# Kernel tuning notes

Hardware: AMD Instinct MI355X
Metric: run time of the kernel (lower is better)

Reference implementation:

```python
import jax, jax.numpy as jnp
import numpy as np

N_CELLS = 500_000
B = 512
D_X = 128
D_Z = 32
D_IN = D_X + D_Z  # 160
H = 256
D_OUT = 16


def _linear_params(key, fan_in, fan_out):
    k1, k2 = jax.random.split(key)
    bound = 1.0 / np.sqrt(fan_in)
    W = jax.random.uniform(k1, (fan_in, fan_out), jnp.float32, -bound, bound)
    b = jax.random.uniform(k2, (fan_out,), jnp.float32, -bound, bound)
    return W, b


def setup_inputs() -> dict:
    key = jax.random.key(0)
    ks = jax.random.split(key, 8)
    X = jax.random.uniform(ks[0], (N_CELLS, D_X), jnp.float32)  # nonneg counts-like
    Z = jax.random.normal(ks[1], (B, D_Z), jnp.float32)
    cell_to_batch = jax.random.randint(ks[2], (N_CELLS,), 0, B, jnp.int64)
    sample_idx_batch = jnp.arange(B, dtype=jnp.int64)
    W1, b1 = _linear_params(ks[3], D_IN, H)
    W2, b2 = _linear_params(ks[4], H, H)
    W3, b3 = _linear_params(ks[5], H, D_OUT)
    return {"X": X, "Z": Z, "W1": W1, "b1": b1, "W2": W2, "b2": b2,
            "W3": W3, "b3": b3, "cell_to_batch": cell_to_batch,
            "sample_idx_batch": sample_idx_batch}


def reference(X, Z, W1, b1, W2, b2, W3, b3, cell_to_batch, sample_idx_batch):
    # gather per-sample covariates to per-cell rows
    Zc = Z[cell_to_batch]                              # [N, D_Z]
    seg = sample_idx_batch[cell_to_batch]              # [N] remapped sample ids
    # preprocessor: log-normalize X, concat covariates
    Xp = jnp.concatenate([jnp.log1p(X), Zc], axis=-1)  # [N, D_IN]
    # cell predictor MLP (Linear-ReLU x2 + Linear)
    h = jax.nn.relu(Xp @ W1 + b1)
    h = jax.nn.relu(h @ W2 + b2)
    X_cell = h @ W3 + b3                               # [N, D_OUT]
    # aggregator: segment mean over cells of each sample
    nseg = sample_idx_batch.shape[0]
    sums = jax.ops.segment_sum(X_cell, seg, num_segments=nseg)
    counts = jax.ops.segment_sum(jnp.ones((X_cell.shape[0], 1), X_cell.dtype), seg, num_segments=nseg)
    Y_sample = sums / jnp.maximum(counts, 1.0)
    # postprocessor: identity
    return Y_sample
```

## Files before the change

kernel.cpp:

```cpp
#include <hip/hip_runtime.h>
#include <hip/hip_bf16.h>

typedef __attribute__((ext_vector_type(8))) short short8;
typedef __attribute__((ext_vector_type(4))) short short4v;
typedef __attribute__((ext_vector_type(4))) float floatx4;

#define N_CELLS  500000
#define B_SAMP   512
#define D_X      128
#define D_Z      32
#define H_DIM    256
#define D_OUT    16

#define M_TILE   128
#define NBLK     3907
#define LDH      264
#define SP_LD    20

#define NREP     64

#define OFF_W1P   0
#define OFF_W2P   65536
#define OFF_W3P   196608
#define OFF_ZW    204800
#define OFF_ACC   729088
#define OFF_CNT   2826240
#define OFF_C2S   2957312

#define W1_BLKS   128
#define W2_BLKS   256
#define W3_BLKS   16
#define ZW_BLKS   512
#define C2S_BLKS  1954

__device__ __forceinline__ short bfb(float x) {
    union { __hip_bfloat16 h; short s; } u;
    u.h = __float2bfloat16(x);
    return u.s;
}
__device__ __forceinline__ int pack2(float a, float b) {
    return ((int)(unsigned short)bfb(a)) | ((int)bfb(b) << 16);
}

__global__ __launch_bounds__(256)
void prep(const float* __restrict__ W1, const float* __restrict__ b1,
          const float* __restrict__ W2, const float* __restrict__ W3,
          const float* __restrict__ Z,
          const int* __restrict__ c2b, const int* __restrict__ sidx,
          __hip_bfloat16* __restrict__ w1p, __hip_bfloat16* __restrict__ w2p,
          __hip_bfloat16* __restrict__ w3p, float* __restrict__ zw1,
          float* __restrict__ cnts, int* __restrict__ c2s) {
    int bid = blockIdx.x;
    int tid = threadIdx.x;
    if (bid < W1_BLKS + W2_BLKS + W3_BLKS) {
        const float* W; __hip_bfloat16* dst; int N, kS, idx; float scale;
        if (bid < W1_BLKS) {
            idx = bid * 256 + tid; W = W1; dst = w1p; N = H_DIM; kS = 4;
            scale = 0.6931471805599453f;
        } else if (bid < W1_BLKS + W2_BLKS) {
            idx = (bid - W1_BLKS) * 256 + tid; W = W2; dst = w2p; N = H_DIM; kS = 8;
            scale = 1.0f;
        } else {
            idx = (bid - W1_BLKS - W2_BLKS) * 256 + tid; W = W3; dst = w3p; N = D_OUT; kS = 8;
            scale = 1.0f;
        }
        int j = idx & 7;
        int L = (idx >> 3) & 63;
        int s = (idx >> 9) % kS;
        int t = idx / (kS << 9);
        int k = s * 32 + ((L >> 4) << 3) + j;
        int n = t * 16 + (L & 15);
        dst[idx] = __float2bfloat16(W[(size_t)k * N + n] * scale);
        return;
    }
    bid -= W1_BLKS + W2_BLKS + W3_BLKS;
    if (bid < ZW_BLKS) {
        int s = bid;
        float a = b1[tid];
        const float* zr = Z + (size_t)s * D_Z;
        const float* wr = W1 + (size_t)D_X * H_DIM + tid;
#pragma unroll 8
        for (int k = 0; k < D_Z; ++k) a += zr[k] * wr[(size_t)k * H_DIM];
        zw1[(size_t)s * H_DIM + tid] = a;
        return;
    }
    bid -= ZW_BLKS;
    int i = bid * 256 + tid;
    if (i < N_CELLS) {
        int si = sidx[c2b[i]];
        c2s[i] = si;
        atomicAdd(&cnts[(size_t)(bid & (NREP - 1)) * B_SAMP + si], 1.0f);
    }
}

__global__ __launch_bounds__(512, 4)
void fused_mlp(const float* __restrict__ X, const int* __restrict__ c2b,
               const int* __restrict__ c2s, const float* __restrict__ b2,
               const float* __restrict__ b3,
               const __hip_bfloat16* __restrict__ w1p,
               const __hip_bfloat16* __restrict__ w2p,
               const __hip_bfloat16* __restrict__ w3p,
               const float* __restrict__ zw1,
               float* __restrict__ accs, float* __restrict__ cnts) {
    __shared__ __align__(16) short sH[M_TILE][LDH];
    __shared__ int sSI[M_TILE];
    float (*sP)[M_TILE][SP_LD] = (float (*)[M_TILE][SP_LD])sH;

    const int tid = threadIdx.x;
    const int w   = tid >> 6;
    const int L   = tid & 63;
    const int q   = L >> 4;
    const int ln  = L & 15;
    const int wm  = w >> 2;
    const int wn  = w & 3;
    const int base = blockIdx.x * M_TILE;

    floatx4 acc[4][4];
#pragma unroll
    for (int mt = 0; mt < 4; ++mt) {
        int g = base + wm * 64 + mt * 16 + ln;
        if (g >= N_CELLS) g = N_CELLS - 1;
        int cbm = c2b[g];
#pragma unroll
        for (int nt = 0; nt < 4; ++nt)
            acc[mt][nt] = *(const floatx4*)(zw1 + (size_t)cbm * H_DIM + wn * 64 + nt * 16 + q * 4);
    }

#pragma unroll
    for (int i = 0; i < 8; ++i) {
        int idx = tid + i * 512;
        int row = idx >> 5, c4 = idx & 31;
        int gr = base + row; if (gr >= N_CELLS) gr = N_CELLS - 1;
        float4 v = *(const float4*)(X + (size_t)gr * D_X + c4 * 4);
        short4v pk;
        pk.x = bfb(__log2f(1.0f + v.x));
        pk.y = bfb(__log2f(1.0f + v.y));
        pk.z = bfb(__log2f(1.0f + v.z));
        pk.w = bfb(__log2f(1.0f + v.w));
        *(short4v*)&sH[row][c4 * 4] = pk;
    }
    if (tid < M_TILE) {
        int gr = base + tid; if (gr >= N_CELLS) gr = N_CELLS - 1;
        sSI[tid] = c2s[gr];
    }
    __syncthreads();

#pragma unroll
    for (int s = 0; s < 4; ++s) {
        short8 xv[4];
#pragma unroll
        for (int mt = 0; mt < 4; ++mt)
            xv[mt] = *(const short8*)&sH[wm * 64 + mt * 16 + ln][s * 32 + q * 8];
#pragma unroll
        for (int nt = 0; nt < 4; ++nt) {
            short8 wf = *(const short8*)(w1p + (size_t)(((((wn * 4 + nt) * 4) + s) << 6) + L) * 8);
#pragma unroll
            for (int mt = 0; mt < 4; ++mt)
                acc[mt][nt] = __builtin_amdgcn_mfma_f32_16x16x32_bf16(wf, xv[mt], acc[mt][nt], 0, 0, 0);
        }
    }
    __syncthreads();
#pragma unroll
    for (int mt = 0; mt < 4; ++mt)
#pragma unroll
        for (int nt = 0; nt < 4; ++nt) {
            short4v pk;
            pk.x = bfb(fmaxf(acc[mt][nt][0], 0.f));
            pk.y = bfb(fmaxf(acc[mt][nt][1], 0.f));
            pk.z = bfb(fmaxf(acc[mt][nt][2], 0.f));
            pk.w = bfb(fmaxf(acc[mt][nt][3], 0.f));
            *(short4v*)&sH[wm * 64 + mt * 16 + ln][wn * 64 + nt * 16 + q * 4] = pk;
        }
    __syncthreads();

#pragma unroll
    for (int nt = 0; nt < 4; ++nt) {
        float4 bv = *(const float4*)(b2 + wn * 64 + nt * 16 + q * 4);
        acc[0][nt] = (floatx4){bv.x, bv.y, bv.z, bv.w};
        acc[1][nt] = acc[0][nt];
        acc[2][nt] = acc[0][nt];
        acc[3][nt] = acc[0][nt];
    }
#pragma unroll
    for (int s = 0; s < 8; ++s) {
        short8 xv[4];
#pragma unroll
        for (int mt = 0; mt < 4; ++mt)
            xv[mt] = *(const short8*)&sH[wm * 64 + mt * 16 + ln][s * 32 + q * 8];
#pragma unroll
        for (int nt = 0; nt < 4; ++nt) {
            short8 wf = *(const short8*)(w2p + (size_t)(((((wn * 4 + nt) * 8) + s) << 6) + L) * 8);
#pragma unroll
            for (int mt = 0; mt < 4; ++mt)
                acc[mt][nt] = __builtin_amdgcn_mfma_f32_16x16x32_bf16(wf, xv[mt], acc[mt][nt], 0, 0, 0);
        }
    }

    int pk[4][4][2];
#pragma unroll
    for (int mt = 0; mt < 4; ++mt)
#pragma unroll
        for (int nt = 0; nt < 4; ++nt) {
            pk[mt][nt][0] = pack2(fmaxf(acc[mt][nt][0], 0.f), fmaxf(acc[mt][nt][1], 0.f));
            pk[mt][nt][1] = pack2(fmaxf(acc[mt][nt][2], 0.f), fmaxf(acc[mt][nt][3], 0.f));
        }
    const int lane0 = (((2 * q) & 3) << 4) + ln;
    const int lane1 = (((2 * q + 1) & 3) << 4) + ln;
    const bool hi = (q >> 1) != 0;
    floatx4 p3[4];
#pragma unroll
    for (int mt = 0; mt < 4; ++mt) p3[mt] = (floatx4){0.f, 0.f, 0.f, 0.f};
#pragma unroll
    for (int h = 0; h < 2; ++h) {
        short8 wf = *(const short8*)(w3p + (size_t)(((2 * wn + h) << 6) + L) * 8);
#pragma unroll
        for (int mt = 0; mt < 4; ++mt) {
            int a0 = __shfl(pk[mt][2 * h][0], lane0);
            int c0 = __shfl(pk[mt][2 * h + 1][0], lane0);
            int a1 = __shfl(pk[mt][2 * h][1], lane0);
            int c1 = __shfl(pk[mt][2 * h + 1][1], lane0);
            int a2 = __shfl(pk[mt][2 * h][0], lane1);
            int c2 = __shfl(pk[mt][2 * h + 1][0], lane1);
            int a3 = __shfl(pk[mt][2 * h][1], lane1);
            int c3 = __shfl(pk[mt][2 * h + 1][1], lane1);
            union { int i[4]; short8 s; } u;
            u.i[0] = hi ? c0 : a0;
            u.i[1] = hi ? c1 : a1;
            u.i[2] = hi ? c2 : a2;
            u.i[3] = hi ? c3 : a3;
            p3[mt] = __builtin_amdgcn_mfma_f32_16x16x32_bf16(wf, u.s, p3[mt], 0, 0, 0);
        }
    }
    __syncthreads();
#pragma unroll
    for (int mt = 0; mt < 4; ++mt)
        *(floatx4*)&sP[wn][wm * 64 + mt * 16 + ln][q * 4] = p3[mt];
    __syncthreads();

    {
        int rep = blockIdx.x & (NREP - 1);
        float* accR = accs + (size_t)rep * (B_SAMP * D_OUT);
#pragma unroll
        for (int i = 0; i < 4; ++i) {
            int idx = tid + i * 512;
            int m = idx >> 4, n = idx & 15;
            int cell = base + m;
            if (cell < N_CELLS) {
                float v = sP[0][m][n] + sP[1][m][n] + sP[2][m][n] + sP[3][m][n] + b3[n];
                atomicAdd(&accR[(size_t)sSI[m] * D_OUT + n], v);
            }
        }
    }
}

__global__ __launch_bounds__(256)
void finalize(const float* __restrict__ accs, const float* __restrict__ cnts,
              float* __restrict__ out) {
    int o = blockIdx.x * blockDim.x + threadIdx.x;
    int s = o >> 4;
    float sum = 0.f, cnt = 0.f;
#pragma unroll 8
    for (int r = 0; r < NREP; ++r) {
        sum += accs[(size_t)r * (B_SAMP * D_OUT) + o];
        cnt += cnts[(size_t)r * B_SAMP + s];
    }
    out[o] = sum / fmaxf(cnt, 1.0f);
}

extern "C" void kernel_launch(void* const* d_in, const int* in_sizes, int n_in,
                              void* d_out, int out_size, void* d_ws, size_t ws_size,
                              hipStream_t stream) {
    const float* X   = (const float*)d_in[0];
    const float* Z   = (const float*)d_in[1];
    const float* W1  = (const float*)d_in[2];
    const float* b1  = (const float*)d_in[3];
    const float* W2  = (const float*)d_in[4];
    const float* b2  = (const float*)d_in[5];
    const float* W3  = (const float*)d_in[6];
    const float* b3  = (const float*)d_in[7];
    const int*   c2b = (const int*)d_in[8];
    const int*   sidx= (const int*)d_in[9];

    char* ws = (char*)d_ws;
    __hip_bfloat16* w1p = (__hip_bfloat16*)(ws + OFF_W1P);
    __hip_bfloat16* w2p = (__hip_bfloat16*)(ws + OFF_W2P);
    __hip_bfloat16* w3p = (__hip_bfloat16*)(ws + OFF_W3P);
    float* zw1  = (float*)(ws + OFF_ZW);
    float* accs = (float*)(ws + OFF_ACC);
    float* cnts = (float*)(ws + OFF_CNT);
    int*   c2s  = (int*)(ws + OFF_C2S);
    float* out  = (float*)d_out;

    hipMemsetAsync(accs, 0, (size_t)NREP * (B_SAMP * D_OUT + B_SAMP) * 4, stream);

    prep<<<W1_BLKS + W2_BLKS + W3_BLKS + ZW_BLKS + C2S_BLKS, 256, 0, stream>>>(
        W1, b1, W2, W3, Z, c2b, sidx, w1p, w2p, w3p, zw1, cnts, c2s);

    fused_mlp<<<NBLK, 512, 0, stream>>>(X, c2b, c2s, b2, b3,
                                        w1p, w2p, w3p, zw1, accs, cnts);
    finalize<<<32, 256, 0, stream>>>(accs, cnts, out);
}
```

Measured before the change: 532.1 us.

## Halve row tile, split hidden columns across waves, and swizzle shared layout

Cuts the cell tile from 128 to 64 rows and gives each of the 8 waves a 32-column slice of the hidden dimension over all rows. Padded shared rows are replaced by an XOR swizzle, and log-normalized inputs go in a separate buffer, so less shared memory is used and one barrier before the layer-1 writeback goes away. The third layer now reads the activations from shared memory with a two-way split-K across waves, replacing the register shuffle packing. This allows more resident blocks, but each cell now pays twice the weight-fragment reloads and twice the block count.

```diff
diff --git a/kernel.cpp b/kernel.cpp
--- a/kernel.cpp
+++ b/kernel.cpp
@@ -12,10 +12,13 @@
 #define H_DIM    256
 #define D_OUT    16
 
-#define M_TILE   128
-#define NBLK     3907
-#define LDH      264
+#define M_TILE   64
+#define NBLK     7813
+#define LDA      128
+#define LDH      256
 #define SP_LD    20
+
+#define SWZ(c, r) ((c) ^ (((r) & 7) << 3))
 
 #define NREP     64
 
@@ -37,9 +40,6 @@
     union { __hip_bfloat16 h; short s; } u;
     u.h = __float2bfloat16(x);
     return u.s;
-}
-__device__ __forceinline__ int pack2(float a, float b) {
-    return ((int)(unsigned short)bfb(a)) | ((int)bfb(b) << 16);
 }
 
 __global__ __launch_bounds__(256)
@@ -102,32 +102,33 @@
                const __hip_bfloat16* __restrict__ w3p,
                const float* __restrict__ zw1,
                float* __restrict__ accs, float* __restrict__ cnts) {
+    __shared__ __align__(16) short sX[M_TILE * LDA];
     __shared__ __align__(16) short sH[M_TILE][LDH];
     __shared__ int sSI[M_TILE];
-    float (*sP)[M_TILE][SP_LD] = (float (*)[M_TILE][SP_LD])sH;
+    short (*xp)[LDA] = (short (*)[LDA])sX;
+    float (*sP)[M_TILE][SP_LD] = (float (*)[M_TILE][SP_LD])sX;
 
     const int tid = threadIdx.x;
     const int w   = tid >> 6;
     const int L   = tid & 63;
     const int q   = L >> 4;
     const int ln  = L & 15;
-    const int wm  = w >> 2;
-    const int wn  = w & 3;
+    const int wn  = w;
     const int base = blockIdx.x * M_TILE;
 
-    floatx4 acc[4][4];
+    floatx4 acc[4][2];
 #pragma unroll
     for (int mt = 0; mt < 4; ++mt) {
-        int g = base + wm * 64 + mt * 16 + ln;
-        if (g >= N_CELLS) g = N_CELLS - 1;
+        int g = base + mt * 16 + ln; if (g >= N_CELLS) g = N_CELLS - 1;
         int cbm = c2b[g];
 #pragma unroll
-        for (int nt = 0; nt < 4; ++nt)
-            acc[mt][nt] = *(const floatx4*)(zw1 + (size_t)cbm * H_DIM + wn * 64 + nt * 16 + q * 4);
-    }
-
-#pragma unroll
-    for (int i = 0; i < 8; ++i) {
+        for (int nt = 0; nt < 2; ++nt)
+            acc[mt][nt] = *(const floatx4*)(zw1 + (size_t)cbm * H_DIM + wn * 32 + nt * 16 + q * 4);
+    }
+    float b3v = b3[tid & 15];
+
+#pragma unroll
+    for (int i = 0; i < 4; ++i) {
         int idx = tid + i * 512;
         int row = idx >> 5, c4 = idx & 31;
         int gr = base + row; if (gr >= N_CELLS) gr = N_CELLS - 1;
@@ -137,7 +138,7 @@
         pk.y = bfb(__log2f(1.0f + v.y));
         pk.z = bfb(__log2f(1.0f + v.z));
         pk.w = bfb(__log2f(1.0f + v.w));
-        *(short4v*)&sH[row][c4 * 4] = pk;
+        *(short4v*)&xp[row][SWZ(c4 * 4, row)] = pk;
     }
     if (tid < M_TILE) {
         int gr = base + tid; if (gr >= N_CELLS) gr = N_CELLS - 1;
@@ -150,103 +151,90 @@
         short8 xv[4];
 #pragma unroll
         for (int mt = 0; mt < 4; ++mt)
-            xv[mt] = *(const short8*)&sH[wm * 64 + mt * 16 + ln][s * 32 + q * 8];
-#pragma unroll
-        for (int nt = 0; nt < 4; ++nt) {
-            short8 wf = *(const short8*)(w1p + (size_t)(((((wn * 4 + nt) * 4) + s) << 6) + L) * 8);
+            xv[mt] = *(const short8*)&xp[mt * 16 + ln][SWZ(s * 32 + q * 8, ln)];
+#pragma unroll
+        for (int nt = 0; nt < 2; ++nt) {
+            int t = wn * 2 + nt;
+            short8 wf = *(const short8*)(w1p + (size_t)(((t * 4 + s) << 6) + L) * 8);
 #pragma unroll
             for (int mt = 0; mt < 4; ++mt)
                 acc[mt][nt] = __builtin_amdgcn_mfma_f32_16x16x32_bf16(wf, xv[mt], acc[mt][nt], 0, 0, 0);
         }
     }
-    __syncthreads();
 #pragma unroll
     for (int mt = 0; mt < 4; ++mt)
 #pragma unroll
-        for (int nt = 0; nt < 4; ++nt) {
+        for (int nt = 0; nt < 2; ++nt) {
             short4v pk;
             pk.x = bfb(fmaxf(acc[mt][nt][0], 0.f));
             pk.y = bfb(fmaxf(acc[mt][nt][1], 0.f));
             pk.z = bfb(fmaxf(acc[mt][nt][2], 0.f));
             pk.w = bfb(fmaxf(acc[mt][nt][3], 0.f));
-            *(short4v*)&sH[wm * 64 + mt * 16 + ln][wn * 64 + nt * 16 + q * 4] = pk;
-        }
-    __syncthreads();
-
-#pragma unroll
-    for (int nt = 0; nt < 4; ++nt) {
-        float4 bv = *(const float4*)(b2 + wn * 64 + nt * 16 + q * 4);
-        acc[0][nt] = (floatx4){bv.x, bv.y, bv.z, bv.w};
-        acc[1][nt] = acc[0][nt];
-        acc[2][nt] = acc[0][nt];
-        acc[3][nt] = acc[0][nt];
+            *(short4v*)&sH[mt * 16 + ln][SWZ(wn * 32 + nt * 16 + q * 4, ln)] = pk;
+        }
+    __syncthreads();
+
+#pragma unroll
+    for (int nt = 0; nt < 2; ++nt) {
+        float4 bv = *(const float4*)(b2 + wn * 32 + nt * 16 + q * 4);
+        floatx4 b = (floatx4){bv.x, bv.y, bv.z, bv.w};
+#pragma unroll
+        for (int mt = 0; mt < 4; ++mt) acc[mt][nt] = b;
     }
 #pragma unroll
     for (int s = 0; s < 8; ++s) {
         short8 xv[4];
 #pragma unroll
         for (int mt = 0; mt < 4; ++mt)
-            xv[mt] = *(const short8*)&sH[wm * 64 + mt * 16 + ln][s * 32 + q * 8];
-#pragma unroll
-        for (int nt = 0; nt < 4; ++nt) {
-            short8 wf = *(const short8*)(w2p + (size_t)(((((wn * 4 + nt) * 8) + s) << 6) + L) * 8);
+            xv[mt] = *(const short8*)&sH[mt * 16 + ln][SWZ(s * 32 + q * 8, ln)];
+#pragma unroll
+        for (int nt = 0; nt < 2; ++nt) {
+            int t = wn * 2 + nt;
+            short8 wf = *(const short8*)(w2p + (size_t)(((t * 8 + s) << 6) + L) * 8);
 #pragma unroll
             for (int mt = 0; mt < 4; ++mt)
                 acc[mt][nt] = __builtin_amdgcn_mfma_f32_16x16x32_bf16(wf, xv[mt], acc[mt][nt], 0, 0, 0);
         }
     }
-
-    int pk[4][4][2];
+    __syncthreads();
 #pragma unroll
     for (int mt = 0; mt < 4; ++mt)
 #pragma unroll
-        for (int nt = 0; nt < 4; ++nt) {
-            pk[mt][nt][0] = pack2(fmaxf(acc[mt][nt][0], 0.f), fmaxf(acc[mt][nt][1], 0.f));
-            pk[mt][nt][1] = pack2(fmaxf(acc[mt][nt][2], 0.f), fmaxf(acc[mt][nt][3], 0.f));
-        }
-    const int lane0 = (((2 * q) & 3) << 4) + ln;
-    const int lane1 = (((2 * q + 1) & 3) << 4) + ln;
-    const bool hi = (q >> 1) != 0;
-    floatx4 p3[4];
-#pragma unroll
-    for (int mt = 0; mt < 4; ++mt) p3[mt] = (floatx4){0.f, 0.f, 0.f, 0.f};
-#pragma unroll
-    for (int h = 0; h < 2; ++h) {
-        short8 wf = *(const short8*)(w3p + (size_t)(((2 * wn + h) << 6) + L) * 8);
-#pragma unroll
-        for (int mt = 0; mt < 4; ++mt) {
-            int a0 = __shfl(pk[mt][2 * h][0], lane0);
-            int c0 = __shfl(pk[mt][2 * h + 1][0], lane0);
-            int a1 = __shfl(pk[mt][2 * h][1], lane0);
-            int c1 = __shfl(pk[mt][2 * h + 1][1], lane0);
-            int a2 = __shfl(pk[mt][2 * h][0], lane1);
-            int c2 = __shfl(pk[mt][2 * h + 1][0], lane1);
-            int a3 = __shfl(pk[mt][2 * h][1], lane1);
-            int c3 = __shfl(pk[mt][2 * h + 1][1], lane1);
-            union { int i[4]; short8 s; } u;
-            u.i[0] = hi ? c0 : a0;
-            u.i[1] = hi ? c1 : a1;
-            u.i[2] = hi ? c2 : a2;
-            u.i[3] = hi ? c3 : a3;
-            p3[mt] = __builtin_amdgcn_mfma_f32_16x16x32_bf16(wf, u.s, p3[mt], 0, 0, 0);
-        }
-    }
-    __syncthreads();
-#pragma unroll
-    for (int mt = 0; mt < 4; ++mt)
-        *(floatx4*)&sP[wn][wm * 64 + mt * 16 + ln][q * 4] = p3[mt];
+        for (int nt = 0; nt < 2; ++nt) {
+            short4v pk;
+            pk.x = bfb(fmaxf(acc[mt][nt][0], 0.f));
+            pk.y = bfb(fmaxf(acc[mt][nt][1], 0.f));
+            pk.z = bfb(fmaxf(acc[mt][nt][2], 0.f));
+            pk.w = bfb(fmaxf(acc[mt][nt][3], 0.f));
+            *(short4v*)&sH[mt * 16 + ln][SWZ(wn * 32 + nt * 16 + q * 4, ln)] = pk;
+        }
+    __syncthreads();
+
+    {
+        int g  = w & 3;
+        int kh = w >> 2;
+        floatx4 a3 = (floatx4){0.f, 0.f, 0.f, 0.f};
+#pragma unroll
+        for (int ss = 0; ss < 4; ++ss) {
+            int s = kh * 4 + ss;
+            short8 hv = *(const short8*)&sH[g * 16 + ln][SWZ(s * 32 + q * 8, ln)];
+            short8 wf = *(const short8*)(w3p + (size_t)((s << 6) + L) * 8);
+            a3 = __builtin_amdgcn_mfma_f32_16x16x32_bf16(wf, hv, a3, 0, 0, 0);
+        }
+        *(floatx4*)&sP[kh][g * 16 + ln][q * 4] = a3;
+    }
     __syncthreads();
 
     {
         int rep = blockIdx.x & (NREP - 1);
         float* accR = accs + (size_t)rep * (B_SAMP * D_OUT);
 #pragma unroll
-        for (int i = 0; i < 4; ++i) {
+        for (int i = 0; i < 2; ++i) {
             int idx = tid + i * 512;
             int m = idx >> 4, n = idx & 15;
             int cell = base + m;
             if (cell < N_CELLS) {
-                float v = sP[0][m][n] + sP[1][m][n] + sP[2][m][n] + sP[3][m][n] + b3[n];
+                float v = sP[0][m][n] + sP[1][m][n] + b3v;
                 atomicAdd(&accR[(size_t)sSI[m] * D_OUT + n], v);
             }
         }
```

After: 467.7 us. -12.1%, faster.
